# Kernel optimization log

Measured on AMD Instinct MI355X. Metric: run time of the kernel, lower is better.

Reference implementation:

```python
import jax, jax.numpy as jnp
import numpy as np

STRIDES = [8, 16, 32, 64, 128]
FEAT_SIZES = [(100, 100), (50, 50), (25, 25), (13, 13), (7, 7)]
IMG_H, IMG_W = 800, 800
NUM_CLASSES = 8  # required by the repeat(8) in _loss_single_scale
BATCH, NUM_GT = 8, 50


def _make_anchor_levels():
    """RetinaNet anchors: octave_base_scale=4, scales_per_octave=3, ratios [0.5,1,2]."""
    ratios = np.array([0.5, 1.0, 2.0], dtype=np.float64)
    scales = 4.0 * 2.0 ** (np.arange(3) / 3.0)
    levels = []
    for stride, (fh, fw) in zip(STRIDES, FEAT_SIZES):
        h_r = np.sqrt(ratios)
        w_r = 1.0 / h_r
        ws = (w_r[:, None] * scales[None, :]).reshape(-1) * stride  # [9]
        hs = (h_r[:, None] * scales[None, :]).reshape(-1) * stride
        base = np.stack([-ws / 2, -hs / 2, ws / 2, hs / 2], axis=1)  # [9,4]
        xs = np.arange(fw) * stride
        ys = np.arange(fh) * stride
        xx, yy = np.meshgrid(xs, ys)  # [fh,fw]
        shifts = np.stack([xx, yy, xx, yy], axis=-1).reshape(-1, 4)  # [fh*fw,4]
        anchors = (shifts[:, None, :] + base[None, :, :]).reshape(-1, 4)  # loc-major, A inner
        levels.append(anchors.astype(np.float32))
    return levels


def _pairwise_iou(a, b):
    # a: [K,4], b: [G,4] -> [K,G]
    area_a = (a[:, 2] - a[:, 0]) * (a[:, 3] - a[:, 1])
    area_b = (b[:, 2] - b[:, 0]) * (b[:, 3] - b[:, 1])
    lt = jnp.maximum(a[:, None, :2], b[None, :, :2])
    rb = jnp.minimum(a[:, None, 2:], b[None, :, 2:])
    wh = jnp.clip(rb - lt, 0.0)
    inter = wh[..., 0] * wh[..., 1]
    return inter / (area_a[:, None] + area_b[None, :] - inter)


def _encode(anchors, gts):
    # DeltaXYWH encode, means=0, stds=1
    aw = anchors[:, 2] - anchors[:, 0]
    ah = anchors[:, 3] - anchors[:, 1]
    ax = anchors[:, 0] + 0.5 * aw
    ay = anchors[:, 1] + 0.5 * ah
    gw = gts[:, 2] - gts[:, 0]
    gh = gts[:, 3] - gts[:, 1]
    gx = gts[:, 0] + 0.5 * gw
    gy = gts[:, 1] + 0.5 * gh
    return jnp.stack([(gx - ax) / aw, (gy - ay) / ah,
                      jnp.log(gw / aw), jnp.log(gh / ah)], axis=1)


def _targets_per_image(anchors, tgt_boxes, tgt_cls):
    # MaxIoUMatcher(thresholds=[0.4,0.5], labels=[0,-1,1], low_quality=True)
    inside = ((anchors[:, 0] >= 0) & (anchors[:, 1] >= 0)
              & (anchors[:, 2] <= IMG_W) & (anchors[:, 3] <= IMG_H))
    iou = _pairwise_iou(anchors, tgt_boxes)             # [K,G]
    iou = jnp.where(inside[:, None], iou, -1.0)          # exclude outside anchors
    max_iou = iou.max(axis=1)
    argmax_gt = iou.argmax(axis=1)
    label = jnp.where(max_iou >= 0.5, 1, jnp.where(max_iou >= 0.4, -1, 0))
    gt_max = iou.max(axis=0)                             # [G]
    is_lq = (iou == gt_max[None, :]) & (gt_max[None, :] > 0)
    any_lq = is_lq.any(axis=1)
    G = tgt_boxes.shape[0]
    lq_gt = jnp.where(is_lq, jnp.arange(G)[None, :], -1).max(axis=1)
    matched_gt = jnp.where(any_lq, lq_gt, argmax_gt)
    label = jnp.where(any_lq, 1, label)
    pos = (label == 1) & inside
    neg = (label == 0) & inside
    deltas = _encode(anchors, tgt_boxes[matched_gt])     # [K,4]
    bbox_targets = jnp.where(pos[:, None], deltas, 0.0)
    bbox_weights = jnp.where(pos[:, None], 1.0, 0.0) * jnp.ones((1, 4), jnp.float32)
    labels_out = jnp.where(pos, tgt_cls[matched_gt].astype(jnp.float32), 0.0)
    label_weights = (pos | neg).astype(jnp.float32)
    return labels_out, label_weights, bbox_targets, bbox_weights, pos.sum(), neg.sum()


def _bce_logits(x, t):
    return jnp.maximum(x, 0.0) - x * t + jnp.log1p(jnp.exp(-jnp.abs(x)))


def _loss_level(cls_out, reg_out, labels, lw, bt, bw, num_samples):
    labels = labels.reshape(-1)
    lw = lw.reshape(-1)
    C = NUM_CLASSES
    cls_score = cls_out.transpose(0, 2, 3, 1).reshape(labels.shape[0], C)  # [N*H*W*A, C]
    tgt = jax.nn.one_hot(labels.astype(jnp.int32), C + 1, dtype=jnp.float32)[:, :C]
    lw2 = jnp.tile(lw, 8).reshape(-1, C)  # faithful to label_weights.repeat(8).reshape(-1, C)
    loss_cls = (_bce_logits(cls_score, tgt) * lw2).sum() / num_samples
    bt = bt.reshape(-1, 4)
    bw = bw.reshape(-1, 4)
    pred = reg_out.transpose(0, 2, 3, 1).reshape(-1, 4)
    loss_bbox = (jnp.abs(pred - bt) * bw).sum() / num_samples
    return loss_cls, loss_bbox


def setup_inputs() -> dict:
    key = jax.random.key(0)
    ks = jax.random.split(key, 16)
    inp = {}
    for i, (fh, fw) in enumerate(FEAT_SIZES):
        inp[f"cls{i}"] = jax.random.normal(ks[i], (BATCH, 9 * NUM_CLASSES, fh, fw), jnp.float32)
        inp[f"reg{i}"] = jax.random.normal(ks[5 + i], (BATCH, 9 * 4, fh, fw), jnp.float32)
    xy = jax.random.uniform(ks[10], (BATCH, NUM_GT, 2), minval=0.0, maxval=600.0)
    wh = jax.random.uniform(ks[11], (BATCH, NUM_GT, 2), minval=20.0, maxval=180.0)
    inp["target_boxes"] = jnp.concatenate([xy, xy + wh], axis=-1).astype(jnp.float32)
    inp["target_class_ids"] = jax.random.randint(ks[12], (BATCH, NUM_GT), 0, NUM_CLASSES, jnp.int64 if jax.config.jax_enable_x64 else jnp.int32)
    return inp


def reference(cls0, cls1, cls2, cls3, cls4, reg0, reg1, reg2, reg3, reg4,
              target_boxes, target_class_ids):
    anchor_levels = _make_anchor_levels()
    anchors = jnp.asarray(np.concatenate(anchor_levels, axis=0))  # [K,4]
    num_lvl = [a.shape[0] for a in anchor_levels]
    labels, lw, bt, bw, npos, nneg = jax.vmap(
        lambda b, c: _targets_per_image(anchors, b, c))(target_boxes, target_class_ids)
    num_samples = (npos.sum() + nneg.sum()).astype(jnp.float32)
    offs = np.cumsum([0] + num_lvl)
    cls_outs = [cls0, cls1, cls2, cls3, cls4]
    reg_outs = [reg0, reg1, reg2, reg3, reg4]
    loss_cls_all = jnp.float32(0.0)
    loss_bbox_all = jnp.float32(0.0)
    for i in range(len(num_lvl)):
        s, e = int(offs[i]), int(offs[i + 1])
        lc, lb = _loss_level(cls_outs[i], reg_outs[i], labels[:, s:e], lw[:, s:e],
                             bt[:, s:e], bw[:, s:e], num_samples)
        loss_cls_all = loss_cls_all + lc
        loss_bbox_all = loss_bbox_all + lb
    return loss_cls_all, loss_bbox_all
```

## Files before the change

kernel.cpp:

```cpp
#include <hip/hip_runtime.h>
#include <cstdint>

#define DEVINL __device__ __forceinline__

constexpr int NB = 8;
constexpr int NG = 50;
constexpr int KTOT = 120087;
constexpr int BK = NB * KTOT;

constexpr int L_W[5]   = {100, 50, 25, 13, 7};
constexpr int L_K[5]   = {90000, 22500, 5625, 1521, 441};
constexpr int L_OFF[5] = {0, 90000, 112500, 118125, 119646};
constexpr int L_STR[5] = {8, 16, 32, 64, 128};
constexpr int L_WSB[5] = {0, 720000, 900000, 945000, 957168};

constexpr double HR_T[3] = {0.7071067811865476, 1.0, 1.4142135623730951};
constexpr double WR_T[3] = {1.0 / HR_T[0], 1.0, 1.0 / HR_T[2]};
constexpr double SC_T[3] = {4.0, 5.039684199579493, 6.3496042078727974};

__device__ float4 g_anc[KTOT];
__device__ double g_accs[256][2];
__device__ unsigned g_ns;
__device__ unsigned g_gtmax[NB * NG];
__device__ int8_t g_lab[BK];
__device__ __align__(8) int8_t g_lw[BK];
__device__ int8_t g_pos[BK];
__device__ int8_t g_mg[BK];

DEVINL unsigned encf(float f) {
  unsigned u = __float_as_uint(f);
  return (u & 0x80000000u) ? ~u : (u | 0x80000000u);
}

DEVINL int lvl_of(int k) {
  return (k < 90000) ? 0 : (k < 112500) ? 1 : (k < 118125) ? 2 : (k < 119646) ? 3 : 4;
}

DEVINL float iou_one(float ax0, float ay0, float ax1, float ay1, float areaA,
                     float bx0, float by0, float bx1, float by1, float areaB) {
  float ltx = fmaxf(ax0, bx0);
  float lty = fmaxf(ay0, by0);
  float rbx = fminf(ax1, bx1);
  float rby = fminf(ay1, by1);
  float wx = fmaxf(rbx - ltx, 0.0f);
  float wy = fmaxf(rby - lty, 0.0f);
  float inter = wx * wy;
  return __fdividef(inter, areaA + areaB - inter);
}

__global__ __launch_bounds__(256) void k_setup() {
  if (blockIdx.x == 0) {
    int t = threadIdx.x;
    g_accs[t][0] = 0.0;
    g_accs[t][1] = 0.0;
    if (t == 0) g_ns = 0u;
  }
  int k = blockIdx.x * 256 + threadIdx.x;
  if (k >= KTOT) return;
  int l = lvl_of(k);
  int r = k - L_OFF[l];
  int loc = r / 9;
  int a = r - loc * 9;
  int W = L_W[l];
  int y = loc / W;
  int x = loc - y * W;
  int st = L_STR[l];
  int ridx = a / 3;
  int sidx = a - ridx * 3;
  double wsz = WR_T[ridx] * SC_T[sidx] * (double)st;
  double hsz = HR_T[ridx] * SC_T[sidx] * (double)st;
  double cx = (double)(x * st);
  double cy = (double)(y * st);
  g_anc[k] = make_float4((float)(cx - wsz * 0.5), (float)(cy - hsz * 0.5),
                         (float)(cx + wsz * 0.5), (float)(cy + hsz * 0.5));
}

DEVINL int axis_cand(int xi, int i0, int lo, int hi, int Wm1) {
  int c;
  if (xi < 4) c = i0 - 1 + xi;
  else if (xi == 4) c = lo;
  else if (xi == 5) c = lo + 1;
  else if (xi == 6) c = hi - 1;
  else if (xi == 7) c = hi;
  else if (xi == 8) c = 0;
  else c = Wm1;
  return min(max(c, 0), Wm1);
}

__global__ __launch_bounds__(256) void k_gtmax2(const float* __restrict__ tb) {
  const int bg = blockIdx.x;
  float4 v = reinterpret_cast<const float4*>(tb)[bg];
  const float bx0 = v.x, by0 = v.y, bx1 = v.z, by1 = v.w;
  const float areaB = (bx1 - bx0) * (by1 - by0);
  const float bcx = 0.5f * (bx0 + bx1), bcy = 0.5f * (by0 + by1);

  float m = -1.0f;
  for (int t = threadIdx.x; t < 4500; t += 256) {
    int l = t / 900;
    int rem = t - l * 900;
    int a = rem / 100;
    int rem2 = rem - a * 100;
    int xi = rem2 / 10;
    int yi = rem2 - xi * 10;
    int W = (l == 0) ? 100 : (l == 1) ? 50 : (l == 2) ? 25 : (l == 3) ? 13 : 7;
    int loff = (l == 0) ? 0 : (l == 1) ? 90000 : (l == 2) ? 112500
               : (l == 3) ? 118125 : 119646;
    float stf = (float)(8 << l);
    float4 A0 = g_anc[loff + a];
    float whalf = -A0.x;
    float hhalf = -A0.y;
    int i0x = (int)floorf(bcx / stf);
    int lox = (int)ceilf(whalf / stf);
    int hix = (int)floorf((800.0f - whalf) / stf);
    int i0y = (int)floorf(bcy / stf);
    int loy = (int)ceilf(hhalf / stf);
    int hiy = (int)floorf((800.0f - hhalf) / stf);
    int cx = axis_cand(xi, i0x, lox, hix, W - 1);
    int cy = axis_cand(yi, i0y, loy, hiy, W - 1);
    int k = loff + (cy * W + cx) * 9 + a;
    float4 A = g_anc[k];
    bool inside = (A.x >= 0.0f) & (A.y >= 0.0f) & (A.z <= 800.0f) & (A.w <= 800.0f);
    float areaA = (A.z - A.x) * (A.w - A.y);
    float iou = inside ? iou_one(A.x, A.y, A.z, A.w, areaA,
                                 bx0, by0, bx1, by1, areaB)
                       : -1.0f;
    m = fmaxf(m, iou);
  }
#pragma unroll
  for (int off = 32; off; off >>= 1) m = fmaxf(m, __shfl_down(m, off));
  __shared__ float s_m[4];
  int lane = threadIdx.x & 63, wid = threadIdx.x >> 6;
  if (lane == 0) s_m[wid] = m;
  __syncthreads();
  if (threadIdx.x == 0) {
    float r = fmaxf(fmaxf(s_m[0], s_m[1]), fmaxf(s_m[2], s_m[3]));
    g_gtmax[bg] = encf(r);
  }
}

constexpr int APB = 4;
__global__ __launch_bounds__(256) void k_assign(const float* __restrict__ tb,
                                                const int* __restrict__ tcls) {
  const int b = blockIdx.y;
  __shared__ float s_b[NG][8];
  __shared__ int s_cls[NG];
  __shared__ unsigned s_cnt;
  int tid = threadIdx.x;
  if (tid == 0) s_cnt = 0u;
  if (tid < NG) {
    float4 v = reinterpret_cast<const float4*>(tb)[b * NG + tid];
    s_b[tid][0] = v.x; s_b[tid][1] = v.y; s_b[tid][2] = v.z; s_b[tid][3] = v.w;
    s_b[tid][4] = (v.z - v.x) * (v.w - v.y);
    unsigned gm = g_gtmax[b * NG + tid];
    s_b[tid][5] = (gm > 0x80000000u) ? __uint_as_float(gm ^ 0x80000000u)
                                     : __uint_as_float(0x7FC00000u);
    s_cls[tid] = tcls[b * NG + tid];
  }
  __syncthreads();

  const int base = (blockIdx.x * 256 + tid) * APB;
  float Ax0[APB], Ay0[APB], Ax1[APB], Ay1[APB], areaA[APB];
  bool inside[APB];
  float ex0 = __builtin_inff(), ey0 = __builtin_inff();
  float ex1 = -__builtin_inff(), ey1 = -__builtin_inff();
#pragma unroll
  for (int ap = 0; ap < APB; ++ap) {
    int k = base + ap;
    bool valid = k < KTOT;
    float4 A = g_anc[valid ? k : 0];
    bool ins = valid & (A.x >= 0.0f) & (A.y >= 0.0f) & (A.z <= 800.0f) & (A.w <= 800.0f);
    inside[ap] = ins;
    ex0 = fminf(ex0, ins ? A.x : __builtin_inff());
    ey0 = fminf(ey0, ins ? A.y : __builtin_inff());
    ex1 = fmaxf(ex1, ins ? A.z : -__builtin_inff());
    ey1 = fmaxf(ey1, ins ? A.w : -__builtin_inff());
    if (!ins) A = make_float4(-4000.0f, -4000.0f, -3999.0f, -3999.0f);
    Ax0[ap] = A.x; Ay0[ap] = A.y; Ax1[ap] = A.z; Ay1[ap] = A.w;
    areaA[ap] = (A.z - A.x) * (A.w - A.y);
  }
#pragma unroll
  for (int off = 1; off < 64; off <<= 1) {
    ex0 = fminf(ex0, __shfl_xor(ex0, off));
    ey0 = fminf(ey0, __shfl_xor(ey0, off));
    ex1 = fmaxf(ex1, __shfl_xor(ex1, off));
    ey1 = fmaxf(ey1, __shfl_xor(ey1, off));
  }

  float best[APB];
  int arg[APB], lqg[APB];
#pragma unroll
  for (int ap = 0; ap < APB; ++ap) { best[ap] = -2.0f; arg[ap] = 0; lqg[ap] = -1; }

  for (int g = 0; g < NG; ++g) {
    float gx0 = s_b[g][0], gy0 = s_b[g][1], gx1 = s_b[g][2], gy1 = s_b[g][3];
    float ox = fminf(ex1, gx1) - fmaxf(ex0, gx0);
    float oy = fminf(ey1, gy1) - fmaxf(ey0, gy0);
    if (ox > 0.0f && oy > 0.0f) {
      float gar = s_b[g][4], qmx = s_b[g][5];
#pragma unroll
      for (int ap = 0; ap < APB; ++ap) {
        float iou = iou_one(Ax0[ap], Ay0[ap], Ax1[ap], Ay1[ap], areaA[ap],
                            gx0, gy0, gx1, gy1, gar);
        if (iou > best[ap]) { best[ap] = iou; arg[ap] = g; }
        if (iou == qmx) lqg[ap] = g;
      }
    }
  }

  int cnt = 0;
#pragma unroll
  for (int ap = 0; ap < APB; ++ap) {
    int k = base + ap;
    if (k < KTOT) {
      int lab = (best[ap] >= 0.5f) ? 1 : ((best[ap] >= 0.4f) ? -1 : 0);
      int mg = arg[ap];
      if (lqg[ap] >= 0) { lab = 1; mg = lqg[ap]; }
      bool pos = (lab == 1) && inside[ap];
      bool neg = (lab == 0) && inside[ap];
      int l = lvl_of(k);
      int r = k - L_OFF[l];
      int widx = L_WSB[l] + b * L_K[l] + r;
      g_lab[widx] = pos ? (int8_t)s_cls[mg] : (int8_t)0;
      g_lw[widx] = (pos || neg) ? 1 : 0;
      g_pos[widx] = pos ? 1 : 0;
      g_mg[widx] = (int8_t)mg;
      cnt += (pos || neg) ? 1 : 0;
    }
  }
#pragma unroll
  for (int off = 32; off; off >>= 1) cnt += __shfl_down(cnt, off);
  if ((tid & 63) == 0 && cnt) atomicAdd(&s_cnt, (unsigned)cnt);
  __syncthreads();
  if (tid == 0 && s_cnt) atomicAdd(&g_ns, s_cnt);
}

template <int HW, int KL, int WSB, int LOFF>
DEVINL void level_term(const float* __restrict__ cls, const float* __restrict__ reg,
                       const float4* __restrict__ tb4, int j, bool valid,
                       float& vc, float& vb) {
  constexpr int NHW9 = 9 * HW;
  int b = j / NHW9;
  int r2 = j - b * NHW9;
  int a = r2 / HW;
  int pix = r2 - a * HW;
  int q = pix * 9 + a;
  int idx = WSB + b * KL + q;

  unsigned long long lwq =
      *reinterpret_cast<const unsigned long long*>(&g_lw[WSB + 8 * q]);
  int lab = g_lab[idx];
  const float* cbase = cls + (b * 72 + a * 8) * HW + pix;
  if (valid && lwq) {
#pragma unroll
    for (int c = 0; c < 8; ++c) {
      float w = (float)((unsigned)(lwq >> (8 * c)) & 0xffu);
      float x = cbase[c * HW];
      float t = (lab == c) ? 1.0f : 0.0f;
      float ax = fabsf(x);
      float e = __expf(-ax);
      float bce = fmaxf(x, 0.0f) - x * t + __logf(1.0f + e);
      vc += bce * w;
    }
  }
  int posb = valid ? g_pos[idx] : 0;
  if (posb) {
    int mg = g_mg[idx];
    float4 A = g_anc[LOFF + q];
    float aw = A.z - A.x, ah = A.w - A.y;
    float acx = A.x + 0.5f * aw, acy = A.y + 0.5f * ah;
    float4 gb = tb4[b * NG + mg];
    float gw = gb.z - gb.x, gh = gb.w - gb.y;
    float gcx = gb.x + 0.5f * gw, gcy = gb.y + 0.5f * gh;
    const float* rbase = reg + (b * 36 + a * 4) * HW + pix;
    vb += fabsf(rbase[0] - (gcx - acx) / aw);
    vb += fabsf(rbase[HW] - (gcy - acy) / ah);
    vb += fabsf(rbase[2 * HW] - logf(gw / aw));
    vb += fabsf(rbase[3 * HW] - logf(gh / ah));
  }
}

__global__ __launch_bounds__(256) void k_loss(
    const float* __restrict__ c0, const float* __restrict__ c1,
    const float* __restrict__ c2, const float* __restrict__ c3,
    const float* __restrict__ c4, const float* __restrict__ r0,
    const float* __restrict__ r1, const float* __restrict__ r2,
    const float* __restrict__ r3, const float* __restrict__ r4,
    const float* __restrict__ tb) {
  const float4* tb4 = reinterpret_cast<const float4*>(tb);
  int T = blockIdx.x * 256 + threadIdx.x;
  bool valid = T < BK;
  int Tc = valid ? T : 0;
  float vc = 0.0f, vb = 0.0f;
  if (Tc < 720000)       level_term<10000, 90000, 0, 0>(c0, r0, tb4, Tc, valid, vc, vb);
  else if (Tc < 900000)  level_term<2500, 22500, 720000, 90000>(c1, r1, tb4, Tc - 720000, valid, vc, vb);
  else if (Tc < 945000)  level_term<625, 5625, 900000, 112500>(c2, r2, tb4, Tc - 900000, valid, vc, vb);
  else if (Tc < 957168)  level_term<169, 1521, 945000, 118125>(c3, r3, tb4, Tc - 945000, valid, vc, vb);
  else                   level_term<49, 441, 957168, 119646>(c4, r4, tb4, Tc - 957168, valid, vc, vb);

#pragma unroll
  for (int off = 32; off; off >>= 1) {
    vc += __shfl_down(vc, off);
    vb += __shfl_down(vb, off);
  }
  __shared__ float sc_[4], sb_[4];
  int lane = threadIdx.x & 63;
  int wid = threadIdx.x >> 6;
  if (lane == 0) { sc_[wid] = vc; sb_[wid] = vb; }
  __syncthreads();
  if (threadIdx.x == 0) {
    float tc = sc_[0] + sc_[1] + sc_[2] + sc_[3];
    float tbx = sb_[0] + sb_[1] + sb_[2] + sb_[3];
    int slot = blockIdx.x & 255;
    if (tc != 0.0f) atomicAdd(&g_accs[slot][0], (double)tc);
    if (tbx != 0.0f) atomicAdd(&g_accs[slot][1], (double)tbx);
  }
}

__global__ __launch_bounds__(256) void k_fin(float* __restrict__ out) {
  int t = threadIdx.x;
  double a0 = g_accs[t][0];
  double a1 = g_accs[t][1];
#pragma unroll
  for (int off = 32; off; off >>= 1) {
    a0 += __shfl_down(a0, off);
    a1 += __shfl_down(a1, off);
  }
  __shared__ double s0[4], s1[4];
  if ((t & 63) == 0) { s0[t >> 6] = a0; s1[t >> 6] = a1; }
  __syncthreads();
  if (t == 0) {
    double A0 = s0[0] + s0[1] + s0[2] + s0[3];
    double A1 = s1[0] + s1[1] + s1[2] + s1[3];
    double n = (double)g_ns;
    out[0] = (float)(A0 / n);
    out[1] = (float)(A1 / n);
  }
}

extern "C" void kernel_launch(void* const* d_in, const int* in_sizes, int n_in,
                              void* d_out, int out_size, void* d_ws, size_t ws_size,
                              hipStream_t stream) {
  const float* c0 = (const float*)d_in[0];
  const float* r0 = (const float*)d_in[1];
  const float* c1 = (const float*)d_in[2];
  const float* r1 = (const float*)d_in[3];
  const float* c2 = (const float*)d_in[4];
  const float* r2 = (const float*)d_in[5];
  const float* c3 = (const float*)d_in[6];
  const float* r3 = (const float*)d_in[7];
  const float* c4 = (const float*)d_in[8];
  const float* r4 = (const float*)d_in[9];
  const float* tb = (const float*)d_in[10];
  const int* tcls = (const int*)d_in[11];
  float* out = (float*)d_out;

  k_setup<<<dim3((KTOT + 255) / 256), dim3(256), 0, stream>>>();
  k_gtmax2<<<dim3(NB * NG), dim3(256), 0, stream>>>(tb);
  k_assign<<<dim3((KTOT + 256 * APB - 1) / (256 * APB), NB), dim3(256), 0, stream>>>(tb, tcls);
  k_loss<<<dim3((BK + 255) / 256), dim3(256), 0, stream>>>(c0, c1, c2, c3, c4, r0, r1, r2,
                                                           r3, r4, tb);
  k_fin<<<dim3(1), dim3(256), 0, stream>>>(out);
}
```

Baseline: 157.3 us.

## Fuse setup/gtmax and loss/finalize kernels, ballot-skip GTs, vectorize loss loads

Merges anchor generation and per-GT max-IoU into one launch by recomputing anchors analytically, which removes the dependency on g_anc. The finalize kernel is folded into k_loss using a last-block-done counter. In k_assign, a wave ballot builds a mask of overlapping GTs so the IoU loop visits only those. k_loss now has each thread handle four pixels with float4 loads of the classification logits, cutting launch count and improving load width. The cost is a more complex tail path and a threadfence/atomic handshake at the end.

```diff
diff --git a/kernel.cpp b/kernel.cpp
--- a/kernel.cpp
+++ b/kernel.cpp
@@ -11,7 +11,6 @@
 constexpr int L_W[5]   = {100, 50, 25, 13, 7};
 constexpr int L_K[5]   = {90000, 22500, 5625, 1521, 441};
 constexpr int L_OFF[5] = {0, 90000, 112500, 118125, 119646};
-constexpr int L_STR[5] = {8, 16, 32, 64, 128};
 constexpr int L_WSB[5] = {0, 720000, 900000, 945000, 957168};
 
 constexpr double HR_T[3] = {0.7071067811865476, 1.0, 1.4142135623730951};
@@ -21,6 +20,7 @@
 __device__ float4 g_anc[KTOT];
 __device__ double g_accs[256][2];
 __device__ unsigned g_ns;
+__device__ unsigned g_done;
 __device__ unsigned g_gtmax[NB * NG];
 __device__ int8_t g_lab[BK];
 __device__ __align__(8) int8_t g_lw[BK];
@@ -31,11 +31,9 @@
   unsigned u = __float_as_uint(f);
   return (u & 0x80000000u) ? ~u : (u | 0x80000000u);
 }
-
 DEVINL int lvl_of(int k) {
   return (k < 90000) ? 0 : (k < 112500) ? 1 : (k < 118125) ? 2 : (k < 119646) ? 3 : 4;
 }
-
 DEVINL float iou_one(float ax0, float ay0, float ax1, float ay1, float areaA,
                      float bx0, float by0, float bx1, float by1, float areaB) {
   float ltx = fmaxf(ax0, bx0);
@@ -48,32 +46,26 @@
   return __fdividef(inter, areaA + areaB - inter);
 }
 
-__global__ __launch_bounds__(256) void k_setup() {
-  if (blockIdx.x == 0) {
-    int t = threadIdx.x;
-    g_accs[t][0] = 0.0;
-    g_accs[t][1] = 0.0;
-    if (t == 0) g_ns = 0u;
-  }
-  int k = blockIdx.x * 256 + threadIdx.x;
-  if (k >= KTOT) return;
-  int l = lvl_of(k);
-  int r = k - L_OFF[l];
-  int loc = r / 9;
-  int a = r - loc * 9;
-  int W = L_W[l];
-  int y = loc / W;
-  int x = loc - y * W;
-  int st = L_STR[l];
-  int ridx = a / 3;
-  int sidx = a - ridx * 3;
-  double wsz = WR_T[ridx] * SC_T[sidx] * (double)st;
-  double hsz = HR_T[ridx] * SC_T[sidx] * (double)st;
-  double cx = (double)(x * st);
-  double cy = (double)(y * st);
-  g_anc[k] = make_float4((float)(cx - wsz * 0.5), (float)(cy - hsz * 0.5),
-                         (float)(cx + wsz * 0.5), (float)(cy + hsz * 0.5));
-}
+DEVINL void wh_f64(int l, int a, double& wsz, double& hsz) {
+  int st = 8 << l;
+  int ridx = a / 3, sidx = a - ridx * 3;
+  double sc = (sidx == 0) ? SC_T[0] : (sidx == 1) ? SC_T[1] : SC_T[2];
+  double wr = (ridx == 0) ? WR_T[0] : (ridx == 1) ? WR_T[1] : WR_T[2];
+  double hr = (ridx == 0) ? HR_T[0] : (ridx == 1) ? HR_T[1] : HR_T[2];
+  wsz = wr * sc * (double)st;
+  hsz = hr * sc * (double)st;
+}
+DEVINL void anchor_from_wh(int l, int xi, int yi, double wsz, double hsz,
+                           float& x0, float& y0, float& x1, float& y1) {
+  int st = 8 << l;
+  double cx = (double)(xi * st), cy = (double)(yi * st);
+  x0 = (float)(cx - wsz * 0.5);
+  y0 = (float)(cy - hsz * 0.5);
+  x1 = (float)(cx + wsz * 0.5);
+  y1 = (float)(cy + hsz * 0.5);
+}
+
+constexpr int NBLK_ANC = (KTOT + 255) / 256;
 
 DEVINL int axis_cand(int xi, int i0, int lo, int hi, int Wm1) {
   int c;
@@ -87,8 +79,31 @@
   return min(max(c, 0), Wm1);
 }
 
-__global__ __launch_bounds__(256) void k_gtmax2(const float* __restrict__ tb) {
-  const int bg = blockIdx.x;
+__global__ __launch_bounds__(256) void k_setup(const float* __restrict__ tb) {
+  if (blockIdx.x < NBLK_ANC) {
+    if (blockIdx.x == 0) {
+      int t = threadIdx.x;
+      g_accs[t][0] = 0.0;
+      g_accs[t][1] = 0.0;
+      if (t == 0) { g_ns = 0u; g_done = 0u; }
+    }
+    int k = blockIdx.x * 256 + threadIdx.x;
+    if (k >= KTOT) return;
+    int l = lvl_of(k);
+    int r = k - L_OFF[l];
+    int loc = r / 9;
+    int a = r - loc * 9;
+    int W = L_W[l];
+    int y = loc / W;
+    int x = loc - y * W;
+    double wsz, hsz;
+    wh_f64(l, a, wsz, hsz);
+    float x0, y0, x1, y1;
+    anchor_from_wh(l, x, y, wsz, hsz, x0, y0, x1, y1);
+    g_anc[k] = make_float4(x0, y0, x1, y1);
+    return;
+  }
+  const int bg = blockIdx.x - NBLK_ANC;
   float4 v = reinterpret_cast<const float4*>(tb)[bg];
   const float bx0 = v.x, by0 = v.y, bx1 = v.z, by1 = v.w;
   const float areaB = (bx1 - bx0) * (by1 - by0);
@@ -103,12 +118,11 @@
     int xi = rem2 / 10;
     int yi = rem2 - xi * 10;
     int W = (l == 0) ? 100 : (l == 1) ? 50 : (l == 2) ? 25 : (l == 3) ? 13 : 7;
-    int loff = (l == 0) ? 0 : (l == 1) ? 90000 : (l == 2) ? 112500
-               : (l == 3) ? 118125 : 119646;
     float stf = (float)(8 << l);
-    float4 A0 = g_anc[loff + a];
-    float whalf = -A0.x;
-    float hhalf = -A0.y;
+    double wsz, hsz;
+    wh_f64(l, a, wsz, hsz);
+    float whalf = (float)(wsz * 0.5);
+    float hhalf = (float)(hsz * 0.5);
     int i0x = (int)floorf(bcx / stf);
     int lox = (int)ceilf(whalf / stf);
     int hix = (int)floorf((800.0f - whalf) / stf);
@@ -117,11 +131,11 @@
     int hiy = (int)floorf((800.0f - hhalf) / stf);
     int cx = axis_cand(xi, i0x, lox, hix, W - 1);
     int cy = axis_cand(yi, i0y, loy, hiy, W - 1);
-    int k = loff + (cy * W + cx) * 9 + a;
-    float4 A = g_anc[k];
-    bool inside = (A.x >= 0.0f) & (A.y >= 0.0f) & (A.z <= 800.0f) & (A.w <= 800.0f);
-    float areaA = (A.z - A.x) * (A.w - A.y);
-    float iou = inside ? iou_one(A.x, A.y, A.z, A.w, areaA,
+    float ax0, ay0, ax1, ay1;
+    anchor_from_wh(l, cx, cy, wsz, hsz, ax0, ay0, ax1, ay1);
+    bool inside = (ax0 >= 0.0f) & (ay0 >= 0.0f) & (ax1 <= 800.0f) & (ay1 <= 800.0f);
+    float areaA = (ax1 - ax0) * (ay1 - ay0);
+    float iou = inside ? iou_one(ax0, ay0, ax1, ay1, areaA,
                                  bx0, by0, bx1, by1, areaB)
                        : -1.0f;
     m = fmaxf(m, iou);
@@ -185,25 +199,34 @@
     ex1 = fmaxf(ex1, __shfl_xor(ex1, off));
     ey1 = fmaxf(ey1, __shfl_xor(ey1, off));
   }
+  unsigned long long amask;
+  {
+    int g = tid & 63;
+    bool act = false;
+    if (g < NG) {
+      float ox = fminf(ex1, s_b[g][2]) - fmaxf(ex0, s_b[g][0]);
+      float oy = fminf(ey1, s_b[g][3]) - fmaxf(ey0, s_b[g][1]);
+      act = (ox > 0.0f) && (oy > 0.0f);
+    }
+    amask = __ballot(act);
+  }
 
   float best[APB];
   int arg[APB], lqg[APB];
 #pragma unroll
   for (int ap = 0; ap < APB; ++ap) { best[ap] = -2.0f; arg[ap] = 0; lqg[ap] = -1; }
 
-  for (int g = 0; g < NG; ++g) {
+  while (amask) {
+    int g = __builtin_ctzll(amask);
+    amask &= amask - 1;
     float gx0 = s_b[g][0], gy0 = s_b[g][1], gx1 = s_b[g][2], gy1 = s_b[g][3];
-    float ox = fminf(ex1, gx1) - fmaxf(ex0, gx0);
-    float oy = fminf(ey1, gy1) - fmaxf(ey0, gy0);
-    if (ox > 0.0f && oy > 0.0f) {
-      float gar = s_b[g][4], qmx = s_b[g][5];
-#pragma unroll
-      for (int ap = 0; ap < APB; ++ap) {
-        float iou = iou_one(Ax0[ap], Ay0[ap], Ax1[ap], Ay1[ap], areaA[ap],
-                            gx0, gy0, gx1, gy1, gar);
-        if (iou > best[ap]) { best[ap] = iou; arg[ap] = g; }
-        if (iou == qmx) lqg[ap] = g;
-      }
+    float gar = s_b[g][4], qmx = s_b[g][5];
+#pragma unroll
+    for (int ap = 0; ap < APB; ++ap) {
+      float iou = iou_one(Ax0[ap], Ay0[ap], Ax1[ap], Ay1[ap], areaA[ap],
+                          gx0, gy0, gx1, gy1, gar);
+      if (iou > best[ap]) { best[ap] = iou; arg[ap] = g; }
+      if (iou == qmx) lqg[ap] = g;
     }
   }
 
@@ -234,48 +257,97 @@
   if (tid == 0 && s_cnt) atomicAdd(&g_ns, s_cnt);
 }
 
-template <int HW, int KL, int WSB, int LOFF>
-DEVINL void level_term(const float* __restrict__ cls, const float* __restrict__ reg,
-                       const float4* __restrict__ tb4, int j, bool valid,
-                       float& vc, float& vb) {
-  constexpr int NHW9 = 9 * HW;
-  int b = j / NHW9;
-  int r2 = j - b * NHW9;
-  int a = r2 / HW;
-  int pix = r2 - a * HW;
-  int q = pix * 9 + a;
-  int idx = WSB + b * KL + q;
-
-  unsigned long long lwq =
-      *reinterpret_cast<const unsigned long long*>(&g_lw[WSB + 8 * q]);
-  int lab = g_lab[idx];
-  const float* cbase = cls + (b * 72 + a * 8) * HW + pix;
-  if (valid && lwq) {
+constexpr int G_OFF[6] = {0, 180000, 225000, 236304, 239400, 240336};
+constexpr int TOTAL_G = 240336;
+
+template <int HW, int GPL, int KL, int WSB, int LOFF>
+DEVINL void level_term4(const float* __restrict__ cls, const float* __restrict__ reg,
+                        const float4* __restrict__ tb4, int j, float& vc, float& vb) {
+  constexpr int NPG = 9 * GPL;
+  int b = j / NPG;
+  int rem = j - b * NPG;
+  int a = rem / GPL;
+  int gi = rem - a * GPL;
+  int pix0 = gi * 4;
+  const float* cb = cls + (b * 72 + a * 8) * HW + pix0;
+  const int8_t* lwb = g_lw + WSB + 8 * (9 * pix0 + a);
+  int idxb = WSB + b * KL + 9 * pix0 + a;
+
+  if (pix0 + 4 <= HW) {
+    float xs[8][4];
 #pragma unroll
     for (int c = 0; c < 8; ++c) {
-      float w = (float)((unsigned)(lwq >> (8 * c)) & 0xffu);
-      float x = cbase[c * HW];
-      float t = (lab == c) ? 1.0f : 0.0f;
-      float ax = fabsf(x);
-      float e = __expf(-ax);
-      float bce = fmaxf(x, 0.0f) - x * t + __logf(1.0f + e);
-      vc += bce * w;
-    }
-  }
-  int posb = valid ? g_pos[idx] : 0;
-  if (posb) {
-    int mg = g_mg[idx];
-    float4 A = g_anc[LOFF + q];
-    float aw = A.z - A.x, ah = A.w - A.y;
-    float acx = A.x + 0.5f * aw, acy = A.y + 0.5f * ah;
-    float4 gb = tb4[b * NG + mg];
-    float gw = gb.z - gb.x, gh = gb.w - gb.y;
-    float gcx = gb.x + 0.5f * gw, gcy = gb.y + 0.5f * gh;
-    const float* rbase = reg + (b * 36 + a * 4) * HW + pix;
-    vb += fabsf(rbase[0] - (gcx - acx) / aw);
-    vb += fabsf(rbase[HW] - (gcy - acy) / ah);
-    vb += fabsf(rbase[2 * HW] - logf(gw / aw));
-    vb += fabsf(rbase[3 * HW] - logf(gh / ah));
+      float4 v4 = *reinterpret_cast<const float4*>(cb + c * HW);
+      xs[c][0] = v4.x; xs[c][1] = v4.y; xs[c][2] = v4.z; xs[c][3] = v4.w;
+    }
+#pragma unroll
+    for (int e = 0; e < 4; ++e) {
+      unsigned long long lwq =
+          *reinterpret_cast<const unsigned long long*>(lwb + 72 * e);
+      if (lwq) {
+        int lab = g_lab[idxb + 9 * e];
+#pragma unroll
+        for (int c = 0; c < 8; ++c) {
+          float w = (float)((unsigned)(lwq >> (8 * c)) & 0xffu);
+          float x = xs[c][e];
+          float t = (lab == c) ? 1.0f : 0.0f;
+          float ax = fabsf(x);
+          float ex = __expf(-ax);
+          vc += (fmaxf(x, 0.0f) - x * t + __logf(1.0f + ex)) * w;
+        }
+      }
+      if (g_pos[idxb + 9 * e]) {
+        int mg = g_mg[idxb + 9 * e];
+        int q = (pix0 + e) * 9 + a;
+        float4 A = g_anc[LOFF + q];
+        float aw = A.z - A.x, ah = A.w - A.y;
+        float acx = A.x + 0.5f * aw, acy = A.y + 0.5f * ah;
+        float4 gb = tb4[b * NG + mg];
+        float gw = gb.z - gb.x, gh = gb.w - gb.y;
+        float gcx = gb.x + 0.5f * gw, gcy = gb.y + 0.5f * gh;
+        const float* rbase = reg + (b * 36 + a * 4) * HW + pix0 + e;
+        vb += fabsf(rbase[0] - (gcx - acx) / aw);
+        vb += fabsf(rbase[HW] - (gcy - acy) / ah);
+        vb += fabsf(rbase[2 * HW] - logf(gw / aw));
+        vb += fabsf(rbase[3 * HW] - logf(gh / ah));
+      }
+    }
+  } else {
+    int nrem = HW - pix0;
+#pragma unroll
+    for (int e = 0; e < 3; ++e) {
+      if (e < nrem) {
+        unsigned long long lwq =
+            *reinterpret_cast<const unsigned long long*>(lwb + 72 * e);
+        if (lwq) {
+          int lab = g_lab[idxb + 9 * e];
+#pragma unroll
+          for (int c = 0; c < 8; ++c) {
+            float w = (float)((unsigned)(lwq >> (8 * c)) & 0xffu);
+            float x = cb[c * HW + e];
+            float t = (lab == c) ? 1.0f : 0.0f;
+            float ax = fabsf(x);
+            float ex = __expf(-ax);
+            vc += (fmaxf(x, 0.0f) - x * t + __logf(1.0f + ex)) * w;
+          }
+        }
+        if (g_pos[idxb + 9 * e]) {
+          int mg = g_mg[idxb + 9 * e];
+          int q = (pix0 + e) * 9 + a;
+          float4 A = g_anc[LOFF + q];
+          float aw = A.z - A.x, ah = A.w - A.y;
+          float acx = A.x + 0.5f * aw, acy = A.y + 0.5f * ah;
+          float4 gb = tb4[b * NG + mg];
+          float gw = gb.z - gb.x, gh = gb.w - gb.y;
+          float gcx = gb.x + 0.5f * gw, gcy = gb.y + 0.5f * gh;
+          const float* rbase = reg + (b * 36 + a * 4) * HW + pix0 + e;
+          vb += fabsf(rbase[0] - (gcx - acx) / aw);
+          vb += fabsf(rbase[HW] - (gcy - acy) / ah);
+          vb += fabsf(rbase[2 * HW] - logf(gw / aw));
+          vb += fabsf(rbase[3 * HW] - logf(gh / ah));
+        }
+      }
+    }
   }
 }
 
@@ -285,24 +357,24 @@
     const float* __restrict__ c4, const float* __restrict__ r0,
     const float* __restrict__ r1, const float* __restrict__ r2,
     const float* __restrict__ r3, const float* __restrict__ r4,
-    const float* __restrict__ tb) {
+    const float* __restrict__ tb, float* __restrict__ out) {
   const float4* tb4 = reinterpret_cast<const float4*>(tb);
   int T = blockIdx.x * 256 + threadIdx.x;
-  bool valid = T < BK;
-  int Tc = valid ? T : 0;
   float vc = 0.0f, vb = 0.0f;
-  if (Tc < 720000)       level_term<10000, 90000, 0, 0>(c0, r0, tb4, Tc, valid, vc, vb);
-  else if (Tc < 900000)  level_term<2500, 22500, 720000, 90000>(c1, r1, tb4, Tc - 720000, valid, vc, vb);
-  else if (Tc < 945000)  level_term<625, 5625, 900000, 112500>(c2, r2, tb4, Tc - 900000, valid, vc, vb);
-  else if (Tc < 957168)  level_term<169, 1521, 945000, 118125>(c3, r3, tb4, Tc - 945000, valid, vc, vb);
-  else                   level_term<49, 441, 957168, 119646>(c4, r4, tb4, Tc - 957168, valid, vc, vb);
-
+  if (T < TOTAL_G) {
+    if (T < G_OFF[1])      level_term4<10000, 2500, 90000, 0, 0>(c0, r0, tb4, T, vc, vb);
+    else if (T < G_OFF[2]) level_term4<2500, 625, 22500, 720000, 90000>(c1, r1, tb4, T - G_OFF[1], vc, vb);
+    else if (T < G_OFF[3]) level_term4<625, 157, 5625, 900000, 112500>(c2, r2, tb4, T - G_OFF[2], vc, vb);
+    else if (T < G_OFF[4]) level_term4<169, 43, 1521, 945000, 118125>(c3, r3, tb4, T - G_OFF[3], vc, vb);
+    else                   level_term4<49, 13, 441, 957168, 119646>(c4, r4, tb4, T - G_OFF[4], vc, vb);
+  }
 #pragma unroll
   for (int off = 32; off; off >>= 1) {
     vc += __shfl_down(vc, off);
     vb += __shfl_down(vb, off);
   }
   __shared__ float sc_[4], sb_[4];
+  __shared__ bool s_last;
   int lane = threadIdx.x & 63;
   int wid = threadIdx.x >> 6;
   if (lane == 0) { sc_[wid] = vc; sb_[wid] = vb; }
@@ -313,27 +385,30 @@
     int slot = blockIdx.x & 255;
     if (tc != 0.0f) atomicAdd(&g_accs[slot][0], (double)tc);
     if (tbx != 0.0f) atomicAdd(&g_accs[slot][1], (double)tbx);
-  }
-}
-
-__global__ __launch_bounds__(256) void k_fin(float* __restrict__ out) {
-  int t = threadIdx.x;
-  double a0 = g_accs[t][0];
-  double a1 = g_accs[t][1];
-#pragma unroll
-  for (int off = 32; off; off >>= 1) {
-    a0 += __shfl_down(a0, off);
-    a1 += __shfl_down(a1, off);
-  }
-  __shared__ double s0[4], s1[4];
-  if ((t & 63) == 0) { s0[t >> 6] = a0; s1[t >> 6] = a1; }
+    __threadfence();
+    unsigned old = atomicAdd(&g_done, 1u);
+    s_last = (old == gridDim.x - 1);
+  }
   __syncthreads();
-  if (t == 0) {
-    double A0 = s0[0] + s0[1] + s0[2] + s0[3];
-    double A1 = s1[0] + s1[1] + s1[2] + s1[3];
-    double n = (double)g_ns;
-    out[0] = (float)(A0 / n);
-    out[1] = (float)(A1 / n);
+  if (s_last) {
+    int t = threadIdx.x;
+    double a0 = atomicAdd(&g_accs[t][0], 0.0);
+    double a1 = atomicAdd(&g_accs[t][1], 0.0);
+#pragma unroll
+    for (int off = 32; off; off >>= 1) {
+      a0 += __shfl_down(a0, off);
+      a1 += __shfl_down(a1, off);
+    }
+    __shared__ double s0[4], s1[4];
+    if (lane == 0) { s0[wid] = a0; s1[wid] = a1; }
+    __syncthreads();
+    if (t == 0) {
+      double A0 = s0[0] + s0[1] + s0[2] + s0[3];
+      double A1 = s1[0] + s1[1] + s1[2] + s1[3];
+      double n = (double)g_ns;
+      out[0] = (float)(A0 / n);
+      out[1] = (float)(A1 / n);
+    }
   }
 }
 
@@ -354,10 +429,8 @@
   const int* tcls = (const int*)d_in[11];
   float* out = (float*)d_out;
 
-  k_setup<<<dim3((KTOT + 255) / 256), dim3(256), 0, stream>>>();
-  k_gtmax2<<<dim3(NB * NG), dim3(256), 0, stream>>>(tb);
+  k_setup<<<dim3(NBLK_ANC + NB * NG), dim3(256), 0, stream>>>(tb);
   k_assign<<<dim3((KTOT + 256 * APB - 1) / (256 * APB), NB), dim3(256), 0, stream>>>(tb, tcls);
-  k_loss<<<dim3((BK + 255) / 256), dim3(256), 0, stream>>>(c0, c1, c2, c3, c4, r0, r1, r2,
-                                                           r3, r4, tb);
-  k_fin<<<dim3(1), dim3(256), 0, stream>>>(out);
-}
+  k_loss<<<dim3((TOTAL_G + 255) / 256), dim3(256), 0, stream>>>(c0, c1, c2, c3, c4,
+                                                                r0, r1, r2, r3, r4, tb, out);
+}
```

Result: slower. 173.2 us (+10.1%).
